# Performance work log

Measured on AMD Instinct MI355X. Metric: run time of the kernel, lower is better.

## Reference

```python
import jax, jax.numpy as jnp
import numpy as np

B = 16384   # tokens
K = 2       # top_k
E = 64      # num_experts
H = 512     # hidden_dim
F = 1024    # expert ffn dim


def setup_inputs() -> dict:
    key = jax.random.key(0)
    k1, k2, k3, k4, k5 = jax.random.split(key, 5)
    hidden_states = jax.random.normal(k1, (B, H), dtype=jnp.float32)
    expert_weights = jax.nn.softmax(jax.random.normal(k2, (B, K), dtype=jnp.float32), axis=-1)
    # Balanced routing: exactly B*K/E assignments per expert (random permutation
    # of a tiled pattern). This is a valid routing for the module and lets the
    # reference use a fixed-capacity grouped GEMM with zero token dropping.
    flat_ids = jax.random.permutation(k3, jnp.tile(jnp.arange(E, dtype=jnp.int32), (B * K) // E))
    expert_ids = flat_ids.reshape(B, K)
    W1 = jax.random.normal(k4, (E, H, F), dtype=jnp.float32) * (1.0 / np.sqrt(H))
    W2 = jax.random.normal(k5, (E, F, H), dtype=jnp.float32) * (1.0 / np.sqrt(F))
    return {"hidden_states": hidden_states, "expert_weights": expert_weights,
            "expert_ids": expert_ids, "W1": W1, "W2": W2}


def reference(hidden_states, expert_weights, expert_ids, W1, W2):
    # Faithful to ExpertGrouping.group_dispatch: every (token, slot) assignment
    # is run through its expert, scaled by its routing weight, and index_add'ed
    # back into the per-token output. Since assignments within an expert are
    # order-independent, we sort assignments by expert id and run one grouped
    # batched GEMM (the fused equivalent of the per-group/per-expert loops).
    b, h = hidden_states.shape
    k = expert_ids.shape[1]
    e = W1.shape[0]
    n = b * k
    cap = n // e  # exact per-expert count (balanced routing)

    flat_ids = expert_ids.reshape(-1)            # [N]
    flat_w = expert_weights.reshape(-1)          # [N]
    token_idx = jnp.arange(n, dtype=jnp.int32) // k  # [N] token for each assignment

    order = jnp.argsort(flat_ids)                # stable sort: groups assignments by expert
    tok_sorted = token_idx[order]                # [N]
    w_sorted = flat_w[order]                     # [N]

    # Gather-dispatch: [E, cap, H]
    xg = hidden_states[tok_sorted].reshape(e, cap, h)
    # Grouped expert FFN (batched over experts)
    hid = jax.nn.silu(jnp.einsum('ech,ehf->ecf', xg, W1))
    yg = jnp.einsum('ecf,efh->ech', hid, W2)     # [E, cap, H]

    # Weighted scatter-combine back to tokens
    weighted = yg.reshape(n, h) * w_sorted[:, None]
    out = jnp.zeros((b, h), dtype=hidden_states.dtype).at[tok_sorted].add(weighted)
    return out
```

## Files before the change

### kernel.cpp

```cpp
#include <hip/hip_runtime.h>
#include <hip/hip_bf16.h>

#define B_TOK 16384
#define TOPK 2
#define NEXP 64
#define HID 512
#define FFN 1024
#define NASSIGN (B_TOK * TOPK)
#define CAP (NASSIGN / NEXP)

typedef unsigned short u16;
typedef __bf16 bf16_t;
typedef bf16_t bf16x8 __attribute__((ext_vector_type(8)));
typedef float f32x4 __attribute__((ext_vector_type(4)));

__device__ __forceinline__ unsigned pkbf(float a, float b) {
  union { bf16_t h[2]; unsigned u; } v;
  v.h[0] = (bf16_t)a; v.h[1] = (bf16_t)b;
  return v.u;
}
__device__ __forceinline__ u16 f2bf(float f) {
  union { bf16_t h; u16 u; } v; v.h = (bf16_t)f; return v.u;
}
__device__ __forceinline__ float bf2f(unsigned u16v) {
  union { unsigned u; float f; } v; v.u = u16v << 16; return v.f;
}

#define GLOAD_LDS16(g, l)                                                     \
  __builtin_amdgcn_global_load_lds((const __attribute__((address_space(1))) void*)(g), \
                                   (__attribute__((address_space(3))) void*)(l), 16, 0, 0)

__global__ void k_route(const int* __restrict__ ids, int* __restrict__ cnt,
                        int* __restrict__ tok_of, int* __restrict__ slot_pos) {
  int n = blockIdx.x * blockDim.x + threadIdx.x;
  if (n >= NASSIGN) return;
  int e = ids[n];
  int r = atomicAdd(&cnt[e], 1);
  int p = e * CAP + r;
  tok_of[p] = n >> 1;
  slot_pos[n] = p;
}

__global__ void k_gather(const float* __restrict__ hs, const int* __restrict__ tok_of,
                         u16* __restrict__ Xg) {
  int p = blockIdx.x * 4 + (threadIdx.x >> 6);
  int lane = threadIdx.x & 63;
  const float4* src = reinterpret_cast<const float4*>(hs + (size_t)tok_of[p] * HID);
  uint2* dst = reinterpret_cast<uint2*>(Xg + (size_t)p * HID);
#pragma unroll
  for (int i = 0; i < 2; i++) {
    float4 v = src[i * 64 + lane];
    uint2 o;
    o.x = pkbf(v.x, v.y);
    o.y = pkbf(v.z, v.w);
    dst[i * 64 + lane] = o;
  }
}

template <int K, int NN, bool SILU>
__global__ __launch_bounds__(256, 4) void k_gemm(const u16* __restrict__ A,
                                                 const float* __restrict__ Wf,
                                                 u16* __restrict__ Cout) {
  constexpr int MT = CAP / 128;
  constexpr int NT = NN / 128;
  constexpr int NWG = NEXP * MT * NT;
  constexpr int Qx = NWG / 8;
  constexpr int KT = K / 32;
  int wg = (blockIdx.x % 8) * Qx + blockIdx.x / 8;
  int e = wg / (MT * NT);
  int rm = wg % (MT * NT);
  int mt = rm / NT, nt = rm % NT;

  const u16* Ab = A + ((size_t)e * CAP + (size_t)mt * 128) * K;

  __shared__ __align__(16) char smc[32768];

  int t_ = threadIdx.x;
  int lane = t_ & 63, wv = t_ >> 6;
  int wm = wv >> 1, wn = wv & 1;
  int l15 = lane & 15, lhi = lane >> 4;

  int pr0 = t_ >> 3, x0 = (t_ & 7) ^ (pr0 & 7);
  int m1 = t_ + 256;
  int pr1 = m1 >> 3, x1 = (m1 & 7) ^ (pr1 & 7);
  const u16* gA0 = Ab + (size_t)(2 * pr0 + (x0 >> 2)) * K + (x0 & 3) * 8;
  const u16* gA1 = Ab + (size_t)(2 * pr1 + (x1 >> 2)) * K + (x1 & 3) * 8;
#define STAGE_A(tn)                                                          \
  do {                                                                       \
    char* d_ = smc + ((tn) & 1) * 8192 + wv * 1024;                          \
    GLOAD_LDS16(gA0 + (size_t)(tn) * 32, d_);                                \
    GLOAD_LDS16(gA1 + (size_t)(tn) * 32, d_ + 4096);                         \
  } while (0)

  int kg = wv;
  const float* gWb = Wf + (size_t)e * K * NN + (size_t)(kg * 8) * NN +
                     (size_t)nt * 128 + lane * 2;
  int wb0 = 16384 + lane * 128 + ((4 * 0 + kg) ^ (lane & 7)) * 16;
  int wb1 = 16384 + lane * 128 + ((4 * 1 + kg) ^ (lane & 7)) * 16;
  float2 L0, L1, L2, L3, L4, L5, L6, L7;
#define LOAD_L(tn)                                                           \
  do {                                                                       \
    const float* g_ = gWb + (size_t)(tn) * 32 * NN;                          \
    L0 = *reinterpret_cast<const float2*>(g_);                               \
    L1 = *reinterpret_cast<const float2*>(g_ + (size_t)1 * NN);              \
    L2 = *reinterpret_cast<const float2*>(g_ + (size_t)2 * NN);              \
    L3 = *reinterpret_cast<const float2*>(g_ + (size_t)3 * NN);              \
    L4 = *reinterpret_cast<const float2*>(g_ + (size_t)4 * NN);              \
    L5 = *reinterpret_cast<const float2*>(g_ + (size_t)5 * NN);              \
    L6 = *reinterpret_cast<const float2*>(g_ + (size_t)6 * NN);              \
    L7 = *reinterpret_cast<const float2*>(g_ + (size_t)7 * NN);              \
  } while (0)
#define WRITE_B(tn)                                                          \
  do {                                                                       \
    char* w_ = smc + ((tn) & 1) * 8192;                                      \
    uint4 v0, v1;                                                            \
    v0.x = pkbf(L0.x, L1.x); v0.y = pkbf(L2.x, L3.x);                        \
    v0.z = pkbf(L4.x, L5.x); v0.w = pkbf(L6.x, L7.x);                        \
    v1.x = pkbf(L0.y, L1.y); v1.y = pkbf(L2.y, L3.y);                        \
    v1.z = pkbf(L4.y, L5.y); v1.w = pkbf(L6.y, L7.y);                        \
    *reinterpret_cast<uint4*>(w_ + wb0) = v0;                                \
    *reinterpret_cast<uint4*>(w_ + wb1) = v1;                                \
  } while (0)

  f32x4 acc[4][4];
#pragma unroll
  for (int i = 0; i < 4; i++)
#pragma unroll
    for (int j = 0; j < 4; j++) {
      f32x4 z = {0.f, 0.f, 0.f, 0.f};
      acc[i][j] = z;
    }
  bf16x8 a[4], b[4];

  int aof[4], bof[4];
#pragma unroll
  for (int f = 0; f < 4; f++) {
    int ar = wm * 64 + f * 16 + l15;
    aof[f] = (ar >> 1) * 128 + (((ar & 1) * 4 + lhi) ^ ((ar >> 1) & 7)) * 16;
    int br = wn * 64 + f * 16 + l15;
    bof[f] = 16384 + (br >> 1) * 128 + (((br & 1) * 4 + lhi) ^ ((br >> 1) & 7)) * 16;
  }

  STAGE_A(0);
  LOAD_L(0);
  WRITE_B(0);
  __syncthreads();

  for (int t = 0; t < KT; t++) {
    const char* pb = smc + (t & 1) * 8192;

    if (t + 1 < KT) LOAD_L(t + 1);
#pragma unroll
    for (int f = 0; f < 4; f++) {
      a[f] = *reinterpret_cast<const bf16x8*>(pb + aof[f]);
      b[f] = *reinterpret_cast<const bf16x8*>(pb + bof[f]);
    }
    if (t + 1 < KT) STAGE_A(t + 1);

#pragma unroll
    for (int mf = 0; mf < 4; mf++)
#pragma unroll
      for (int nf = 0; nf < 4; nf++)
        acc[mf][nf] = __builtin_amdgcn_mfma_f32_16x16x32_bf16(a[mf], b[nf], acc[mf][nf], 0, 0, 0);

    if (t + 1 < KT) WRITE_B(t + 1);
    __syncthreads();
  }
#undef STAGE_A
#undef LOAD_L
#undef WRITE_B

#pragma unroll
  for (int mf = 0; mf < 4; mf++) {
#pragma unroll
    for (int nf = 0; nf < 4; nf++) {
#pragma unroll
      for (int rg = 0; rg < 4; rg++) {
        float v = acc[mf][nf][rg];
        int grow = mt * 128 + wm * 64 + mf * 16 + lhi * 4 + rg;
        int gcol = nt * 128 + wn * 64 + nf * 16 + l15;
        size_t off = ((size_t)e * CAP + grow) * NN + gcol;
        if constexpr (SILU) v = v / (1.0f + __expf(-v));
        Cout[off] = f2bf(v);
      }
    }
  }
}

__global__ void k_combine(const u16* __restrict__ yws, const int* __restrict__ slot_pos,
                          const float* __restrict__ w, float* __restrict__ out) {
  int tk = blockIdx.x * 4 + (threadIdx.x >> 6);
  int lane = threadIdx.x & 63;
  int p0 = slot_pos[2 * tk], p1 = slot_pos[2 * tk + 1];
  float w0 = w[2 * tk], w1 = w[2 * tk + 1];
  uint4 ua = reinterpret_cast<const uint4*>(yws + (size_t)p0 * HID)[lane];
  uint4 ub = reinterpret_cast<const uint4*>(yws + (size_t)p1 * HID)[lane];
  float4 o0, o1;
  o0.x = w0 * bf2f(ua.x & 0xffffu) + w1 * bf2f(ub.x & 0xffffu);
  o0.y = w0 * bf2f(ua.x >> 16) + w1 * bf2f(ub.x >> 16);
  o0.z = w0 * bf2f(ua.y & 0xffffu) + w1 * bf2f(ub.y & 0xffffu);
  o0.w = w0 * bf2f(ua.y >> 16) + w1 * bf2f(ub.y >> 16);
  o1.x = w0 * bf2f(ua.z & 0xffffu) + w1 * bf2f(ub.z & 0xffffu);
  o1.y = w0 * bf2f(ua.z >> 16) + w1 * bf2f(ub.z >> 16);
  o1.z = w0 * bf2f(ua.w & 0xffffu) + w1 * bf2f(ub.w & 0xffffu);
  o1.w = w0 * bf2f(ua.w >> 16) + w1 * bf2f(ub.w >> 16);
  float4* dst = reinterpret_cast<float4*>(out + (size_t)tk * HID + lane * 8);
  dst[0] = o0;
  dst[1] = o1;
}

extern "C" void kernel_launch(void* const* d_in, const int* in_sizes, int n_in,
                              void* d_out, int out_size, void* d_ws, size_t ws_size,
                              hipStream_t stream) {
  const float* hs = (const float*)d_in[0];
  const float* wts = (const float*)d_in[1];
  const int* ids = (const int*)d_in[2];
  const float* W1 = (const float*)d_in[3];
  const float* W2 = (const float*)d_in[4];
  float* out = (float*)d_out;

  char* ws = (char*)d_ws;
  size_t o = 0;
  int* cnt = (int*)(ws + o);       o += 1024;
  int* slot_pos = (int*)(ws + o);  o += (size_t)NASSIGN * 4;
  int* tok_of = (int*)(ws + o);    o += (size_t)NASSIGN * 4;
  o = (o + 255) & ~(size_t)255;
  u16* Xg = (u16*)(ws + o);        o += (size_t)NASSIGN * HID * 2;
  u16* hid = (u16*)(ws + o);       o += (size_t)NASSIGN * FFN * 2;
  u16* yws = (u16*)(ws + o);       o += (size_t)NASSIGN * HID * 2;

  hipMemsetAsync(cnt, 0, NEXP * sizeof(int), stream);
  k_route<<<(NASSIGN + 255) / 256, 256, 0, stream>>>(ids, cnt, tok_of, slot_pos);
  k_gather<<<NASSIGN / 4, 256, 0, stream>>>(hs, tok_of, Xg);
  k_gemm<HID, FFN, true><<<NEXP * (CAP / 128) * (FFN / 128), 256, 0, stream>>>(Xg, W1, hid);
  k_gemm<FFN, HID, false><<<NEXP * (CAP / 128) * (HID / 128), 256, 0, stream>>>(hid, W2, yws);
  k_combine<<<B_TOK / 4, 256, 0, stream>>>(yws, slot_pos, wts, out);
}
```

Baseline: 256.2 us.

## Double-buffer weight register loads two tiles ahead with manual waitcnt barriers

The fp32 weight tile loads in the grouped GEMM now alternate between two register sets and are issued two k-tiles ahead, with the loop unrolled by two. Conversion and the LDS write for the next tile move ahead of the MFMA block. The full __syncthreads is replaced with explicit s_waitcnt vmcnt(8)/lgkmcnt(0) plus s_barrier and a scheduling barrier, so the newest global loads stay in flight across the barrier. The aim is to hide global-load latency behind the MFMAs, at the cost of more registers and an assumption that KT is even.

After: 760.0 us. +196.6%, slower.

```diff
diff --git a/kernel.cpp b/kernel.cpp
--- a/kernel.cpp
+++ b/kernel.cpp
@@ -95,29 +95,29 @@
   int kg = wv;
   const float* gWb = Wf + (size_t)e * K * NN + (size_t)(kg * 8) * NN +
                      (size_t)nt * 128 + lane * 2;
-  int wb0 = 16384 + lane * 128 + ((4 * 0 + kg) ^ (lane & 7)) * 16;
-  int wb1 = 16384 + lane * 128 + ((4 * 1 + kg) ^ (lane & 7)) * 16;
-  float2 L0, L1, L2, L3, L4, L5, L6, L7;
-#define LOAD_L(tn)                                                           \
+  int wb0 = 16384 + lane * 128 + ((kg) ^ (lane & 7)) * 16;
+  int wb1 = 16384 + lane * 128 + ((4 + kg) ^ (lane & 7)) * 16;
+  float2 LA[8], LB[8];
+#define LOAD_L(P, tn)                                                        \
   do {                                                                       \
     const float* g_ = gWb + (size_t)(tn) * 32 * NN;                          \
-    L0 = *reinterpret_cast<const float2*>(g_);                               \
-    L1 = *reinterpret_cast<const float2*>(g_ + (size_t)1 * NN);              \
-    L2 = *reinterpret_cast<const float2*>(g_ + (size_t)2 * NN);              \
-    L3 = *reinterpret_cast<const float2*>(g_ + (size_t)3 * NN);              \
-    L4 = *reinterpret_cast<const float2*>(g_ + (size_t)4 * NN);              \
-    L5 = *reinterpret_cast<const float2*>(g_ + (size_t)5 * NN);              \
-    L6 = *reinterpret_cast<const float2*>(g_ + (size_t)6 * NN);              \
-    L7 = *reinterpret_cast<const float2*>(g_ + (size_t)7 * NN);              \
-  } while (0)
-#define WRITE_B(tn)                                                          \
+    P[0] = *reinterpret_cast<const float2*>(g_);                             \
+    P[1] = *reinterpret_cast<const float2*>(g_ + (size_t)1 * NN);            \
+    P[2] = *reinterpret_cast<const float2*>(g_ + (size_t)2 * NN);            \
+    P[3] = *reinterpret_cast<const float2*>(g_ + (size_t)3 * NN);            \
+    P[4] = *reinterpret_cast<const float2*>(g_ + (size_t)4 * NN);            \
+    P[5] = *reinterpret_cast<const float2*>(g_ + (size_t)5 * NN);            \
+    P[6] = *reinterpret_cast<const float2*>(g_ + (size_t)6 * NN);            \
+    P[7] = *reinterpret_cast<const float2*>(g_ + (size_t)7 * NN);            \
+  } while (0)
+#define WRITE_B(P, tn)                                                       \
   do {                                                                       \
     char* w_ = smc + ((tn) & 1) * 8192;                                      \
     uint4 v0, v1;                                                            \
-    v0.x = pkbf(L0.x, L1.x); v0.y = pkbf(L2.x, L3.x);                        \
-    v0.z = pkbf(L4.x, L5.x); v0.w = pkbf(L6.x, L7.x);                        \
-    v1.x = pkbf(L0.y, L1.y); v1.y = pkbf(L2.y, L3.y);                        \
-    v1.z = pkbf(L4.y, L5.y); v1.w = pkbf(L6.y, L7.y);                        \
+    v0.x = pkbf(P[0].x, P[1].x); v0.y = pkbf(P[2].x, P[3].x);                \
+    v0.z = pkbf(P[4].x, P[5].x); v0.w = pkbf(P[6].x, P[7].x);                \
+    v1.x = pkbf(P[0].y, P[1].y); v1.y = pkbf(P[2].y, P[3].y);                \
+    v1.z = pkbf(P[4].y, P[5].y); v1.w = pkbf(P[6].y, P[7].y);                \
     *reinterpret_cast<uint4*>(w_ + wb0) = v0;                                \
     *reinterpret_cast<uint4*>(w_ + wb1) = v1;                                \
   } while (0)
@@ -141,31 +141,45 @@
     bof[f] = 16384 + (br >> 1) * 128 + (((br & 1) * 4 + lhi) ^ ((br >> 1) & 7)) * 16;
   }
 
+#define ITER(t, SETW, SETL)                                                  \
+  do {                                                                       \
+    const char* pb = smc + ((t) & 1) * 8192;                                 \
+    _Pragma("unroll") for (int f = 0; f < 4; f++) {                          \
+      a[f] = *reinterpret_cast<const bf16x8*>(pb + aof[f]);                  \
+      b[f] = *reinterpret_cast<const bf16x8*>(pb + bof[f]);                  \
+    }                                                                        \
+    if ((t) + 1 < KT) {                                                      \
+      STAGE_A((t) + 1);                                                      \
+      WRITE_B(SETW, (t) + 1);                 \
+    }                                                                        \
+    if ((t) + 2 < KT) LOAD_L(SETL, (t) + 2);                                 \
+    _Pragma("unroll") for (int mf = 0; mf < 4; mf++)                         \
+        _Pragma("unroll") for (int nf = 0; nf < 4; nf++)                     \
+            acc[mf][nf] = __builtin_amdgcn_mfma_f32_16x16x32_bf16(           \
+                a[mf], b[nf], acc[mf][nf], 0, 0, 0);                         \
+    if ((t) + 2 < KT)                                                        \
+      asm volatile("s_waitcnt vmcnt(8) lgkmcnt(0)" ::: "memory");            \
+    else                                                                     \
+      asm volatile("s_waitcnt vmcnt(0) lgkmcnt(0)" ::: "memory");            \
+    __builtin_amdgcn_sched_barrier(0);                                       \
+    __builtin_amdgcn_s_barrier();                                            \
+  } while (0)
+
   STAGE_A(0);
-  LOAD_L(0);
-  WRITE_B(0);
-  __syncthreads();
-
-  for (int t = 0; t < KT; t++) {
-    const char* pb = smc + (t & 1) * 8192;
-
-    if (t + 1 < KT) LOAD_L(t + 1);
-#pragma unroll
-    for (int f = 0; f < 4; f++) {
-      a[f] = *reinterpret_cast<const bf16x8*>(pb + aof[f]);
-      b[f] = *reinterpret_cast<const bf16x8*>(pb + bof[f]);
-    }
-    if (t + 1 < KT) STAGE_A(t + 1);
-
-#pragma unroll
-    for (int mf = 0; mf < 4; mf++)
-#pragma unroll
-      for (int nf = 0; nf < 4; nf++)
-        acc[mf][nf] = __builtin_amdgcn_mfma_f32_16x16x32_bf16(a[mf], b[nf], acc[mf][nf], 0, 0, 0);
-
-    if (t + 1 < KT) WRITE_B(t + 1);
-    __syncthreads();
-  }
+  LOAD_L(LA, 0);
+  asm volatile("s_waitcnt vmcnt(0)" ::: "memory");
+  __builtin_amdgcn_sched_barrier(0);
+  WRITE_B(LA, 0);
+  LOAD_L(LB, 1);
+  asm volatile("s_waitcnt lgkmcnt(0)" ::: "memory");
+  __builtin_amdgcn_sched_barrier(0);
+  __builtin_amdgcn_s_barrier();
+
+  for (int tt = 0; tt < KT; tt += 2) {
+    ITER(tt, LB, LA);
+    ITER(tt + 1, LA, LB);
+  }
+#undef ITER
 #undef STAGE_A
 #undef LOAD_L
 #undef WRITE_B
```

## Enlarge GEMM tile to 256 rows with 512 threads and explicit waitcnt pipelining

Applied to the files above, without the earlier changes.

The grouped GEMM now uses 512-thread blocks computing 256x128 tiles, so each fp32 weight tile is loaded and converted to bf16 once for twice as many token rows. The weight staging is rewritten so each thread loads one column across 8 k-rows, and the separate A and B LDS regions grow to 48KB. __syncthreads is replaced with manual s_waitcnt, sched_barrier and s_barrier to overlap the next tile's loads with MFMA work. Larger blocks and more LDS may lower occupancy, and the hand-placed wait counts depend on exact instruction counts.

New measurement: 230.9 us. 9.9% less time.

```diff
diff --git a/kernel.cpp b/kernel.cpp
--- a/kernel.cpp
+++ b/kernel.cpp
@@ -58,22 +58,22 @@
 }
 
 template <int K, int NN, bool SILU>
-__global__ __launch_bounds__(256, 4) void k_gemm(const u16* __restrict__ A,
+__global__ __launch_bounds__(512, 4) void k_gemm(const u16* __restrict__ A,
                                                  const float* __restrict__ Wf,
                                                  u16* __restrict__ Cout) {
-  constexpr int MT = CAP / 128;
+  constexpr int MT = CAP / 256;
   constexpr int NT = NN / 128;
   constexpr int NWG = NEXP * MT * NT;
-  constexpr int Qx = NWG / 8;
+  constexpr int Q = NWG / 8;
   constexpr int KT = K / 32;
-  int wg = (blockIdx.x % 8) * Qx + blockIdx.x / 8;
+  int wg = (blockIdx.x % 8) * Q + blockIdx.x / 8;
   int e = wg / (MT * NT);
   int rm = wg % (MT * NT);
   int mt = rm / NT, nt = rm % NT;
 
-  const u16* Ab = A + ((size_t)e * CAP + (size_t)mt * 128) * K;
-
-  __shared__ __align__(16) char smc[32768];
+  const u16* Ab = A + ((size_t)e * CAP + (size_t)mt * 256) * K;
+
+  __shared__ __align__(16) char smc[49152];
 
   int t_ = threadIdx.x;
   int lane = t_ & 63, wv = t_ >> 6;
@@ -81,45 +81,32 @@
   int l15 = lane & 15, lhi = lane >> 4;
 
   int pr0 = t_ >> 3, x0 = (t_ & 7) ^ (pr0 & 7);
-  int m1 = t_ + 256;
-  int pr1 = m1 >> 3, x1 = (m1 & 7) ^ (pr1 & 7);
   const u16* gA0 = Ab + (size_t)(2 * pr0 + (x0 >> 2)) * K + (x0 & 3) * 8;
-  const u16* gA1 = Ab + (size_t)(2 * pr1 + (x1 >> 2)) * K + (x1 & 3) * 8;
+  const u16* gA1 = gA0 + (size_t)128 * K;
 #define STAGE_A(tn)                                                          \
   do {                                                                       \
-    char* d_ = smc + ((tn) & 1) * 8192 + wv * 1024;                          \
+    char* d_ = smc + ((tn) & 1) * 16384 + wv * 1024;                         \
     GLOAD_LDS16(gA0 + (size_t)(tn) * 32, d_);                                \
-    GLOAD_LDS16(gA1 + (size_t)(tn) * 32, d_ + 4096);                         \
-  } while (0)
-
-  int kg = wv;
+    GLOAD_LDS16(gA1 + (size_t)(tn) * 32, d_ + 8192);                         \
+  } while (0)
+
+  int ncol = t_ & 127, kg = t_ >> 7;
   const float* gWb = Wf + (size_t)e * K * NN + (size_t)(kg * 8) * NN +
-                     (size_t)nt * 128 + lane * 2;
-  int wb0 = 16384 + lane * 128 + ((4 * 0 + kg) ^ (lane & 7)) * 16;
-  int wb1 = 16384 + lane * 128 + ((4 * 1 + kg) ^ (lane & 7)) * 16;
-  float2 L0, L1, L2, L3, L4, L5, L6, L7;
+                     (size_t)nt * 128 + ncol;
+  int wbo = (ncol >> 1) * 128 + ((((ncol & 1) * 4 + kg) ^ ((ncol >> 1) & 7)) << 4);
+  float L[8];
 #define LOAD_L(tn)                                                           \
   do {                                                                       \
     const float* g_ = gWb + (size_t)(tn) * 32 * NN;                          \
-    L0 = *reinterpret_cast<const float2*>(g_);                               \
-    L1 = *reinterpret_cast<const float2*>(g_ + (size_t)1 * NN);              \
-    L2 = *reinterpret_cast<const float2*>(g_ + (size_t)2 * NN);              \
-    L3 = *reinterpret_cast<const float2*>(g_ + (size_t)3 * NN);              \
-    L4 = *reinterpret_cast<const float2*>(g_ + (size_t)4 * NN);              \
-    L5 = *reinterpret_cast<const float2*>(g_ + (size_t)5 * NN);              \
-    L6 = *reinterpret_cast<const float2*>(g_ + (size_t)6 * NN);              \
-    L7 = *reinterpret_cast<const float2*>(g_ + (size_t)7 * NN);              \
+    _Pragma("unroll") for (int j = 0; j < 8; j++) L[j] = g_[(size_t)j * NN]; \
   } while (0)
 #define WRITE_B(tn)                                                          \
   do {                                                                       \
-    char* w_ = smc + ((tn) & 1) * 8192;                                      \
-    uint4 v0, v1;                                                            \
-    v0.x = pkbf(L0.x, L1.x); v0.y = pkbf(L2.x, L3.x);                        \
-    v0.z = pkbf(L4.x, L5.x); v0.w = pkbf(L6.x, L7.x);                        \
-    v1.x = pkbf(L0.y, L1.y); v1.y = pkbf(L2.y, L3.y);                        \
-    v1.z = pkbf(L4.y, L5.y); v1.w = pkbf(L6.y, L7.y);                        \
-    *reinterpret_cast<uint4*>(w_ + wb0) = v0;                                \
-    *reinterpret_cast<uint4*>(w_ + wb1) = v1;                                \
+    char* w_ = smc + 32768 + ((tn) & 1) * 8192;                              \
+    uint4 v;                                                                 \
+    v.x = pkbf(L[0], L[1]); v.y = pkbf(L[2], L[3]);                          \
+    v.z = pkbf(L[4], L[5]); v.w = pkbf(L[6], L[7]);                          \
+    *reinterpret_cast<uint4*>(w_ + wbo) = v;                                 \
   } while (0)
 
   f32x4 acc[4][4];
@@ -136,39 +123,59 @@
 #pragma unroll
   for (int f = 0; f < 4; f++) {
     int ar = wm * 64 + f * 16 + l15;
-    aof[f] = (ar >> 1) * 128 + (((ar & 1) * 4 + lhi) ^ ((ar >> 1) & 7)) * 16;
+    aof[f] = (ar >> 1) * 128 + ((((ar & 1) * 4 + lhi) ^ ((ar >> 1) & 7)) << 4);
     int br = wn * 64 + f * 16 + l15;
-    bof[f] = 16384 + (br >> 1) * 128 + (((br & 1) * 4 + lhi) ^ ((br >> 1) & 7)) * 16;
-  }
+    bof[f] = (br >> 1) * 128 + ((((br & 1) * 4 + lhi) ^ ((br >> 1) & 7)) << 4);
+  }
+
+#define LGKM0()                                                              \
+  do {                                                                       \
+    asm volatile("s_waitcnt lgkmcnt(0)" ::: "memory");                       \
+    __builtin_amdgcn_sched_barrier(0);                                       \
+  } while (0)
 
   STAGE_A(0);
   LOAD_L(0);
+  asm volatile("s_waitcnt vmcnt(0)" ::: "memory");
+  __builtin_amdgcn_sched_barrier(0);
   WRITE_B(0);
-  __syncthreads();
+  LGKM0();
+  __builtin_amdgcn_s_barrier();
 
   for (int t = 0; t < KT; t++) {
-    const char* pb = smc + (t & 1) * 8192;
-
-    if (t + 1 < KT) LOAD_L(t + 1);
+    const char* pA = smc + (t & 1) * 16384;
+    const char* pB = smc + 32768 + (t & 1) * 8192;
+
+    if (t + 1 < KT) {
+      LOAD_L(t + 1);
+      STAGE_A(t + 1);
+    }
+
 #pragma unroll
     for (int f = 0; f < 4; f++) {
-      a[f] = *reinterpret_cast<const bf16x8*>(pb + aof[f]);
-      b[f] = *reinterpret_cast<const bf16x8*>(pb + bof[f]);
-    }
-    if (t + 1 < KT) STAGE_A(t + 1);
-
+      a[f] = *reinterpret_cast<const bf16x8*>(pA + aof[f]);
+      b[f] = *reinterpret_cast<const bf16x8*>(pB + bof[f]);
+    }
+    LGKM0();
 #pragma unroll
     for (int mf = 0; mf < 4; mf++)
 #pragma unroll
       for (int nf = 0; nf < 4; nf++)
         acc[mf][nf] = __builtin_amdgcn_mfma_f32_16x16x32_bf16(a[mf], b[nf], acc[mf][nf], 0, 0, 0);
 
-    if (t + 1 < KT) WRITE_B(t + 1);
-    __syncthreads();
+    if (t + 1 < KT) {
+      asm volatile("s_waitcnt vmcnt(4)" ::: "memory");
+      __builtin_amdgcn_sched_barrier(0);
+      WRITE_B(t + 1);
+      asm volatile("s_waitcnt vmcnt(0) lgkmcnt(0)" ::: "memory");
+      __builtin_amdgcn_sched_barrier(0);
+      __builtin_amdgcn_s_barrier();
+    }
   }
 #undef STAGE_A
 #undef LOAD_L
 #undef WRITE_B
+#undef LGKM0
 
 #pragma unroll
   for (int mf = 0; mf < 4; mf++) {
@@ -177,7 +184,7 @@
 #pragma unroll
       for (int rg = 0; rg < 4; rg++) {
         float v = acc[mf][nf][rg];
-        int grow = mt * 128 + wm * 64 + mf * 16 + lhi * 4 + rg;
+        int grow = mt * 256 + wm * 64 + mf * 16 + lhi * 4 + rg;
         int gcol = nt * 128 + wn * 64 + nf * 16 + l15;
         size_t off = ((size_t)e * CAP + grow) * NN + gcol;
         if constexpr (SILU) v = v / (1.0f + __expf(-v));
@@ -232,7 +239,7 @@
   hipMemsetAsync(cnt, 0, NEXP * sizeof(int), stream);
   k_route<<<(NASSIGN + 255) / 256, 256, 0, stream>>>(ids, cnt, tok_of, slot_pos);
   k_gather<<<NASSIGN / 4, 256, 0, stream>>>(hs, tok_of, Xg);
-  k_gemm<HID, FFN, true><<<NEXP * (CAP / 128) * (FFN / 128), 256, 0, stream>>>(Xg, W1, hid);
-  k_gemm<FFN, HID, false><<<NEXP * (CAP / 128) * (HID / 128), 256, 0, stream>>>(hid, W2, yws);
+  k_gemm<HID, FFN, true><<<NEXP * (CAP / 256) * (FFN / 128), 512, 0, stream>>>(Xg, W1, hid);
+  k_gemm<FFN, HID, false><<<NEXP * (CAP / 256) * (HID / 128), 512, 0, stream>>>(hid, W2, yws);
   k_combine<<<B_TOK / 4, 256, 0, stream>>>(yws, slot_pos, wts, out);
 }
```
